# Kernel optimization log

Measured on AMD Instinct MI355X. Metric: run time of the kernel, lower is better.

The kernel has to match this reference:

```python
import jax, jax.numpy as jnp
import numpy as np

N_QUBITS = 10
N_LAYERS = 4
BATCH = 8192
DIM = 2 ** N_QUBITS


def setup_inputs() -> dict:
    key = jax.random.key(0)
    k1, k2 = jax.random.split(key)
    x = jax.random.normal(k1, (BATCH, N_QUBITS), dtype=jnp.float32)
    weights = jax.random.normal(k2, (N_LAYERS, N_QUBITS, 3), dtype=jnp.float32) * 0.1
    return {"x": x, "weights": weights}


def _apply_1q(state, U, q):
    """Apply shared 2x2 gate U to qubit q (wire 0 = most significant bit)."""
    B = state.shape[0]
    s = state.reshape(B, 2 ** q, 2, -1)
    s = jnp.einsum('ij,bajc->baic', U, s)
    return s.reshape(B, -1)


def _apply_1q_batched(state, U, q):
    """Apply per-sample 2x2 gates U[b] to qubit q."""
    B = state.shape[0]
    s = state.reshape(B, 2 ** q, 2, -1)
    s = jnp.einsum('bij,bajc->baic', U, s)
    return s.reshape(B, -1)


def _apply_cnot(state, c, t):
    """CNOT with control c, target t."""
    B = state.shape[0]
    s = state.reshape((B,) + (2,) * N_QUBITS)
    c_ax, t_ax = c + 1, t + 1
    ctrl0 = jnp.take(s, 0, axis=c_ax)
    ctrl1 = jnp.take(s, 1, axis=c_ax)
    # after removing control axis, target axis shifts down if it was after control
    t_ax2 = t_ax - 1 if t_ax > c_ax else t_ax
    ctrl1 = jnp.flip(ctrl1, axis=t_ax2)  # X on target when control=1
    s = jnp.stack([ctrl0, ctrl1], axis=c_ax)
    return s.reshape(B, -1)


def _rot_matrix(phi, theta, omega):
    """PennyLane Rot(phi,theta,omega) = RZ(omega) RY(theta) RZ(phi)."""
    c = jnp.cos(theta / 2)
    s = jnp.sin(theta / 2)
    e = lambda a: jnp.exp(1j * a)
    row0 = jnp.stack([e(-(phi + omega) / 2) * c, -e((phi - omega) / 2) * s])
    row1 = jnp.stack([e(-(phi - omega) / 2) * s, e((phi + omega) / 2) * c])
    return jnp.stack([row0, row1]).astype(jnp.complex64)


def _circuit(x, weights):
    B = x.shape[0]
    state = jnp.zeros((B, DIM), jnp.complex64).at[:, 0].set(1.0)
    # angle encoding: RY(x[:, q]) on each wire, batched over samples
    for q in range(N_QUBITS):
        a = x[:, q] / 2
        c, s = jnp.cos(a), jnp.sin(a)
        U = jnp.stack([jnp.stack([c, -s], -1), jnp.stack([s, c], -1)], -2)
        state = _apply_1q_batched(state, U.astype(jnp.complex64), q)
    for l in range(N_LAYERS):
        for q in range(N_QUBITS):
            U = _rot_matrix(weights[l, q, 0], weights[l, q, 1], weights[l, q, 2])
            state = _apply_1q(state, U, q)
        for q in range(N_QUBITS - 1):
            state = _apply_cnot(state, q, q + 1)
        if N_QUBITS > 2:
            state = _apply_cnot(state, N_QUBITS - 1, 0)
    # <Z_q> = sum_{bit_q=0} |amp|^2 - sum_{bit_q=1} |amp|^2
    probs = jnp.real(state) ** 2 + jnp.imag(state) ** 2
    outs = []
    for q in range(N_QUBITS):
        p = probs.reshape(B, 2 ** q, 2, -1)
        outs.append(p[:, :, 0, :].sum((1, 2)) - p[:, :, 1, :].sum((1, 2)))
    return jnp.stack(outs, axis=-1)  # [B, n_qubits]


def reference(x, weights):
    return _circuit(x, weights)
```

## Files before the change

### kernel.cpp

```cpp
#include <hip/hip_runtime.h>
#include <math.h>

#define NQ 10
#define NL 4

typedef float v2f __attribute__((ext_vector_type(2)));

template<int CTRL>
__device__ __forceinline__ float dppx(float v) {
  return __int_as_float(__builtin_amdgcn_update_dpp(0, __float_as_int(v), CTRL, 0xF, 0xF, true));
}
template<int OFF>
__device__ __forceinline__ float swzx(float v) {
  return __int_as_float(__builtin_amdgcn_ds_swizzle(__float_as_int(v), OFF));
}
__device__ __forceinline__ void pl16swap(float &a, float &b) {
  asm("v_permlane16_swap_b32 %0, %1" : "+v"(a), "+v"(b));
}
__device__ __forceinline__ void pl32swap(float &a, float &b) {
  asm("v_permlane32_swap_b32 %0, %1" : "+v"(a), "+v"(b));
}

template<int LB>
__device__ __forceinline__ float part(float v) {
  if constexpr (LB == 0) return dppx<0xB1>(v);
  else if constexpr (LB == 1) return dppx<0x4E>(v);
  else if constexpr (LB == 2) return swzx<0x101F>(v);
  else return swzx<0x201F>(v);
}

__device__ __forceinline__ v2f cmul(v2f u, v2f a) {
  v2f d;
  asm("v_pk_mul_f32 %0, %1, %2 op_sel_hi:[0,1]\n\t"
      "v_pk_fma_f32 %0, %1, %2, %0 op_sel:[1,1,0] op_sel_hi:[1,0,1] neg_lo:[0,1,0]"
      : "=&v"(d) : "v"(u), "v"(a));
  return d;
}
__device__ __forceinline__ void cfma(v2f &d, v2f u, v2f a) {
  asm("v_pk_fma_f32 %0, %1, %2, %0 op_sel_hi:[0,1,1]\n\t"
      "v_pk_fma_f32 %0, %1, %2, %0 op_sel:[1,1,0] op_sel_hi:[1,0,1] neg_lo:[0,1,0]"
      : "+v"(d) : "v"(u), "v"(a));
}

template<int RB>
__device__ __forceinline__ void gate_rbit(v2f a[16], v2f u00, v2f u01, v2f u10, v2f u11) {
#pragma unroll
  for (int r0 = 0; r0 < 16; ++r0) {
    if ((r0 >> RB) & 1) continue;
    const int r1 = r0 | (1 << RB);
    const v2f a0 = a[r0], a1 = a[r1];
    v2f n0 = cmul(u00, a0); cfma(n0, u01, a1);
    v2f n1 = cmul(u10, a0); cfma(n1, u11, a1);
    a[r0] = n0;
    a[r1] = n1;
  }
}

template<int LB>
__device__ __forceinline__ void gate_part(v2f a[16], v2f cS, v2f cP) {
#pragma unroll
  for (int h = 0; h < 4; ++h) {
    v2f p[4];
#pragma unroll
    for (int k = 0; k < 4; ++k) {
      const int r = h * 4 + k;
      p[k].x = part<LB>(a[r].x);
      p[k].y = part<LB>(a[r].y);
    }
#pragma unroll
    for (int k = 0; k < 4; ++k) {
      const int r = h * 4 + k;
      v2f n = cmul(cS, a[r]); cfma(n, cP, p[k]);
      a[r] = n;
    }
  }
}

template<bool IS32>
__device__ __forceinline__ void gate_swap(v2f a[16], v2f cL, v2f cH) {
#pragma unroll
  for (int r = 0; r < 16; ++r) {
    float lx = a[r].x, hx = a[r].x;
    float ly = a[r].y, hy = a[r].y;
    if constexpr (IS32) { pl32swap(lx, hx); pl32swap(ly, hy); }
    else                { pl16swap(lx, hx); pl16swap(ly, hy); }
    v2f lo, hi;
    lo.x = lx; lo.y = ly;
    hi.x = hx; hi.y = hy;
    v2f n = cmul(cL, lo); cfma(n, cH, hi);
    a[r] = n;
  }
}

__device__ __forceinline__ void ring_comp(v2f a[16], int addr0, int addr1, bool odd) {
  float B[16];
#pragma unroll
  for (int g = 0; g < 16; ++g) {
    const int par = ((g ^ (g >> 1) ^ (g >> 2) ^ (g >> 3)) & 1);
    B[g] = __int_as_float(__builtin_amdgcn_ds_bpermute(par ? addr1 : addr0,
                                                       __float_as_int(a[g].x)));
  }
#pragma unroll
  for (int r = 0; r < 16; ++r) {
    const int g = (r ^ (r >> 1));
    a[r].x = odd ? B[g ^ 12] : B[g];
  }
#pragma unroll
  for (int g = 0; g < 16; ++g) {
    const int par = ((g ^ (g >> 1) ^ (g >> 2) ^ (g >> 3)) & 1);
    B[g] = __int_as_float(__builtin_amdgcn_ds_bpermute(par ? addr1 : addr0,
                                                       __float_as_int(a[g].y)));
  }
#pragma unroll
  for (int r = 0; r < 16; ++r) {
    const int g = (r ^ (r >> 1));
    a[r].y = odd ? B[g ^ 12] : B[g];
  }
}

__device__ __forceinline__ float wsum(float v) {
  v += dppx<0xB1>(v);
  v += dppx<0x4E>(v);
  v += swzx<0x101F>(v);
  v += swzx<0x201F>(v);
  { float a = v, b = v; pl16swap(a, b); v = a + b; }
  { float a = v, b = v; pl32swap(a, b); v = a + b; }
  return v;
}

__device__ __forceinline__ void encode(const float* __restrict__ xb, int lane, v2f a[16]) {
  float lfac;
  {
    float c, s;
    sincosf(0.5f * xb[9], &s, &c); lfac  = ((lane >> 0) & 1) ? s : c;
    sincosf(0.5f * xb[8], &s, &c); lfac *= ((lane >> 1) & 1) ? s : c;
    sincosf(0.5f * xb[7], &s, &c); lfac *= ((lane >> 2) & 1) ? s : c;
    sincosf(0.5f * xb[6], &s, &c); lfac *= ((lane >> 3) & 1) ? s : c;
    sincosf(0.5f * xb[5], &s, &c); lfac *= ((lane >> 4) & 1) ? s : c;
    sincosf(0.5f * xb[4], &s, &c); lfac *= ((lane >> 5) & 1) ? s : c;
  }
  float c0, s0, c1, s1, c2, s2, c3, s3;
  sincosf(0.5f * xb[0], &s0, &c0);
  sincosf(0.5f * xb[1], &s1, &c1);
  sincosf(0.5f * xb[2], &s2, &c2);
  sincosf(0.5f * xb[3], &s3, &c3);
#pragma unroll
  for (int r = 0; r < 16; ++r) {
    float f = lfac;
    f *= ((r >> 0) & 1) ? s3 : c3;
    f *= ((r >> 1) & 1) ? s2 : c2;
    f *= ((r >> 2) & 1) ? s1 : c1;
    f *= ((r >> 3) & 1) ? s0 : c0;
    a[r].x = f;
    a[r].y = 0.f;
  }
}

__device__ __forceinline__ void measure(const v2f a[16], int lane, float z[NQ]) {
  float p[16];
#pragma unroll
  for (int r = 0; r < 16; ++r) p[r] = a[r].x * a[r].x + a[r].y * a[r].y;
#pragma unroll
  for (int q = 0; q < 4; ++q) {
    const int rb = 3 - q;
    float acc = 0.f;
#pragma unroll
    for (int r = 0; r < 16; ++r) acc += ((r >> rb) & 1) ? -p[r] : p[r];
    z[q] = acc;
  }
  float P = 0.f;
#pragma unroll
  for (int r = 0; r < 16; ++r) P += p[r];
#pragma unroll
  for (int q = 4; q < NQ; ++q) {
    const int lb = 9 - q;
    z[q] = ((lane >> lb) & 1) ? -P : P;
  }
#pragma unroll
  for (int q = 0; q < NQ; ++q) z[q] = wsum(z[q]);
}

__global__ __launch_bounds__(256) void qsim_kernel(const float* __restrict__ x,
                                                   const float* __restrict__ w,
                                                   float* __restrict__ out,
                                                   int batch) {
  __shared__ __align__(16) float gsh[NL * NQ * 8];
  const int tid = threadIdx.x;
  if (tid < NL * NQ) {
    const float phi = w[tid * 3 + 0];
    const float th  = w[tid * 3 + 1];
    const float om  = w[tid * 3 + 2];
    float c, s, cp, sp, cm, sm;
    sincosf(0.5f * th, &s, &c);
    sincosf(-0.5f * (phi + om), &sp, &cp);
    sincosf(0.5f * (phi - om), &sm, &cm);
    float* g = &gsh[tid * 8];
    g[0] = cp * c;  g[1] = sp * c;
    g[2] = -cm * s; g[3] = -sm * s;
    g[4] = cm * s;  g[5] = -sm * s;
    g[6] = cp * c;  g[7] = -sp * c;
  }
  __syncthreads();

  const int samp = (int)(blockIdx.x * (blockDim.x >> 6)) + (tid >> 6);
  const int lane = tid & 63;
  if (samp >= batch) return;

  const int addr0 = 4 * (lane ^ (lane >> 1));
  const int addr1 = addr0 ^ 128;
  const bool lodd = (lane & 1);

  v2f a[16];
  encode(x + samp * NQ, lane, a);

#pragma unroll
  for (int l = 0; l < NL; ++l) {
    const float* gl = &gsh[l * NQ * 8];

#pragma unroll
    for (int q = 0; q < 4; ++q) {
      const v2f* gv = (const v2f*)(gl + q * 8);
      const v2f u00 = gv[0], u01 = gv[1], u10 = gv[2], u11 = gv[3];
      if (q == 0)      gate_rbit<3>(a, u00, u01, u10, u11);
      else if (q == 1) gate_rbit<2>(a, u00, u01, u10, u11);
      else if (q == 2) gate_rbit<1>(a, u00, u01, u10, u11);
      else             gate_rbit<0>(a, u00, u01, u10, u11);
    }
    {
      const v2f* gv = (const v2f*)(gl + 4 * 8);
      const bool hb = (lane >> 5) & 1;
      const v2f cL = hb ? gv[2] : gv[0];
      const v2f cH = hb ? gv[3] : gv[1];
      gate_swap<true>(a, cL, cH);
    }
    {
      const v2f* gv = (const v2f*)(gl + 5 * 8);
      const bool hb = (lane >> 4) & 1;
      const v2f cL = hb ? gv[2] : gv[0];
      const v2f cH = hb ? gv[3] : gv[1];
      gate_swap<false>(a, cL, cH);
    }
#pragma unroll
    for (int q = 6; q < 10; ++q) {
      const v2f* gv = (const v2f*)(gl + q * 8);
      const bool hb = (lane >> (9 - q)) & 1;
      const v2f cS = hb ? gv[3] : gv[0];
      const v2f cP = hb ? gv[2] : gv[1];
      if (q == 6)      gate_part<3>(a, cS, cP);
      else if (q == 7) gate_part<2>(a, cS, cP);
      else if (q == 8) gate_part<1>(a, cS, cP);
      else             gate_part<0>(a, cS, cP);
    }

    ring_comp(a, addr0, addr1, lodd);
  }

  float z[NQ];
  measure(a, lane, z);

  if (lane == 0) {
#pragma unroll
    for (int q = 0; q < NQ; ++q) out[samp * NQ + q] = z[q];
  }
}

extern "C" void kernel_launch(void* const* d_in, const int* in_sizes, int n_in,
                              void* d_out, int out_size, void* d_ws, size_t ws_size,
                              hipStream_t stream) {
  const float* x = (const float*)d_in[0];
  const float* w = (const float*)d_in[1];
  float* out = (float*)d_out;
  const int batch = in_sizes[0] / NQ;
  const int waves_per_block = 256 / 64;
  const int grid = (batch + waves_per_block - 1) / waves_per_block;
  hipLaunchKernelGGL(qsim_kernel, dim3(grid), dim3(256), 0, stream, x, w, out, batch);
}
```

Before: 137.5 us.

## Precompute gates in separate kernel, use fast trig, merge lane-bit reductions

Moves the weight-to-gate-matrix computation into a tiny separate kernel that writes a global device array, so the main kernel no longer needs shared memory or __syncthreads and each block skips the redundant setup. Replaces sincosf with the fast __sinf/__cosf intrinsics in encoding and gate preparation. Replaces six separate wave reductions for the lane-bit qubits with a single butterfly reduction whose signed FMAs leave each qubit's expectation in a power-of-two lane. The trade-offs are reduced trig precision, an extra kernel launch, and gate coefficients now read from global memory instead of LDS.

New measurement: 147.1 us. 1.07x slower.

```diff
diff --git a/kernel.cpp b/kernel.cpp
--- a/kernel.cpp
+++ b/kernel.cpp
@@ -5,6 +5,8 @@
 #define NL 4
 
 typedef float v2f __attribute__((ext_vector_type(2)));
+
+__device__ float g_gates[NL * NQ * 8];
 
 template<int CTRL>
 __device__ __forceinline__ float dppx(float v) {
@@ -131,19 +133,19 @@
 __device__ __forceinline__ void encode(const float* __restrict__ xb, int lane, v2f a[16]) {
   float lfac;
   {
-    float c, s;
-    sincosf(0.5f * xb[9], &s, &c); lfac  = ((lane >> 0) & 1) ? s : c;
-    sincosf(0.5f * xb[8], &s, &c); lfac *= ((lane >> 1) & 1) ? s : c;
-    sincosf(0.5f * xb[7], &s, &c); lfac *= ((lane >> 2) & 1) ? s : c;
-    sincosf(0.5f * xb[6], &s, &c); lfac *= ((lane >> 3) & 1) ? s : c;
-    sincosf(0.5f * xb[5], &s, &c); lfac *= ((lane >> 4) & 1) ? s : c;
-    sincosf(0.5f * xb[4], &s, &c); lfac *= ((lane >> 5) & 1) ? s : c;
-  }
-  float c0, s0, c1, s1, c2, s2, c3, s3;
-  sincosf(0.5f * xb[0], &s0, &c0);
-  sincosf(0.5f * xb[1], &s1, &c1);
-  sincosf(0.5f * xb[2], &s2, &c2);
-  sincosf(0.5f * xb[3], &s3, &c3);
+    float c, s, h;
+    h = 0.5f * xb[9]; s = __sinf(h); c = __cosf(h); lfac  = ((lane >> 0) & 1) ? s : c;
+    h = 0.5f * xb[8]; s = __sinf(h); c = __cosf(h); lfac *= ((lane >> 1) & 1) ? s : c;
+    h = 0.5f * xb[7]; s = __sinf(h); c = __cosf(h); lfac *= ((lane >> 2) & 1) ? s : c;
+    h = 0.5f * xb[6]; s = __sinf(h); c = __cosf(h); lfac *= ((lane >> 3) & 1) ? s : c;
+    h = 0.5f * xb[5]; s = __sinf(h); c = __cosf(h); lfac *= ((lane >> 4) & 1) ? s : c;
+    h = 0.5f * xb[4]; s = __sinf(h); c = __cosf(h); lfac *= ((lane >> 5) & 1) ? s : c;
+  }
+  const float h0 = 0.5f * xb[0], h1 = 0.5f * xb[1], h2 = 0.5f * xb[2], h3 = 0.5f * xb[3];
+  const float s0 = __sinf(h0), c0 = __cosf(h0);
+  const float s1 = __sinf(h1), c1 = __cosf(h1);
+  const float s2 = __sinf(h2), c2 = __cosf(h2);
+  const float s3 = __sinf(h3), c3 = __cosf(h3);
 #pragma unroll
   for (int r = 0; r < 16; ++r) {
     float f = lfac;
@@ -156,52 +158,27 @@
   }
 }
 
-__device__ __forceinline__ void measure(const v2f a[16], int lane, float z[NQ]) {
-  float p[16];
-#pragma unroll
-  for (int r = 0; r < 16; ++r) p[r] = a[r].x * a[r].x + a[r].y * a[r].y;
-#pragma unroll
-  for (int q = 0; q < 4; ++q) {
-    const int rb = 3 - q;
-    float acc = 0.f;
-#pragma unroll
-    for (int r = 0; r < 16; ++r) acc += ((r >> rb) & 1) ? -p[r] : p[r];
-    z[q] = acc;
-  }
-  float P = 0.f;
-#pragma unroll
-  for (int r = 0; r < 16; ++r) P += p[r];
-#pragma unroll
-  for (int q = 4; q < NQ; ++q) {
-    const int lb = 9 - q;
-    z[q] = ((lane >> lb) & 1) ? -P : P;
-  }
-#pragma unroll
-  for (int q = 0; q < NQ; ++q) z[q] = wsum(z[q]);
-}
-
-__global__ __launch_bounds__(256) void qsim_kernel(const float* __restrict__ x,
-                                                   const float* __restrict__ w,
-                                                   float* __restrict__ out,
-                                                   int batch) {
-  __shared__ __align__(16) float gsh[NL * NQ * 8];
-  const int tid = threadIdx.x;
-  if (tid < NL * NQ) {
-    const float phi = w[tid * 3 + 0];
-    const float th  = w[tid * 3 + 1];
-    const float om  = w[tid * 3 + 2];
-    float c, s, cp, sp, cm, sm;
-    sincosf(0.5f * th, &s, &c);
-    sincosf(-0.5f * (phi + om), &sp, &cp);
-    sincosf(0.5f * (phi - om), &sm, &cm);
-    float* g = &gsh[tid * 8];
+__global__ void prep_gates(const float* __restrict__ w) {
+  const int t = threadIdx.x;
+  if (t < NL * NQ) {
+    const float phi = w[t * 3 + 0];
+    const float th  = w[t * 3 + 1];
+    const float om  = w[t * 3 + 2];
+    const float c  = __cosf(0.5f * th),          s  = __sinf(0.5f * th);
+    const float cp = __cosf(-0.5f * (phi + om)), sp = __sinf(-0.5f * (phi + om));
+    const float cm = __cosf(0.5f * (phi - om)),  sm = __sinf(0.5f * (phi - om));
+    float* g = g_gates + t * 8;
     g[0] = cp * c;  g[1] = sp * c;
     g[2] = -cm * s; g[3] = -sm * s;
     g[4] = cm * s;  g[5] = -sm * s;
     g[6] = cp * c;  g[7] = -sp * c;
   }
-  __syncthreads();
-
+}
+
+__global__ __launch_bounds__(256) void qsim_kernel(const float* __restrict__ x,
+                                                   float* __restrict__ out,
+                                                   int batch) {
+  const int tid = threadIdx.x;
   const int samp = (int)(blockIdx.x * (blockDim.x >> 6)) + (tid >> 6);
   const int lane = tid & 63;
   if (samp >= batch) return;
@@ -215,37 +192,44 @@
 
 #pragma unroll
   for (int l = 0; l < NL; ++l) {
-    const float* gl = &gsh[l * NQ * 8];
+    const float* gl = g_gates + l * NQ * 8;
 
 #pragma unroll
     for (int q = 0; q < 4; ++q) {
-      const v2f* gv = (const v2f*)(gl + q * 8);
-      const v2f u00 = gv[0], u01 = gv[1], u10 = gv[2], u11 = gv[3];
+      const float* g = gl + q * 8;
+      const v2f u00 = {g[0], g[1]}, u01 = {g[2], g[3]};
+      const v2f u10 = {g[4], g[5]}, u11 = {g[6], g[7]};
       if (q == 0)      gate_rbit<3>(a, u00, u01, u10, u11);
       else if (q == 1) gate_rbit<2>(a, u00, u01, u10, u11);
       else if (q == 2) gate_rbit<1>(a, u00, u01, u10, u11);
       else             gate_rbit<0>(a, u00, u01, u10, u11);
     }
     {
-      const v2f* gv = (const v2f*)(gl + 4 * 8);
+      const float* g = gl + 4 * 8;
       const bool hb = (lane >> 5) & 1;
-      const v2f cL = hb ? gv[2] : gv[0];
-      const v2f cH = hb ? gv[3] : gv[1];
+      const v2f u00 = {g[0], g[1]}, u01 = {g[2], g[3]};
+      const v2f u10 = {g[4], g[5]}, u11 = {g[6], g[7]};
+      const v2f cL = hb ? u10 : u00;
+      const v2f cH = hb ? u11 : u01;
       gate_swap<true>(a, cL, cH);
     }
     {
-      const v2f* gv = (const v2f*)(gl + 5 * 8);
+      const float* g = gl + 5 * 8;
       const bool hb = (lane >> 4) & 1;
-      const v2f cL = hb ? gv[2] : gv[0];
-      const v2f cH = hb ? gv[3] : gv[1];
+      const v2f u00 = {g[0], g[1]}, u01 = {g[2], g[3]};
+      const v2f u10 = {g[4], g[5]}, u11 = {g[6], g[7]};
+      const v2f cL = hb ? u10 : u00;
+      const v2f cH = hb ? u11 : u01;
       gate_swap<false>(a, cL, cH);
     }
 #pragma unroll
     for (int q = 6; q < 10; ++q) {
-      const v2f* gv = (const v2f*)(gl + q * 8);
+      const float* g = gl + q * 8;
       const bool hb = (lane >> (9 - q)) & 1;
-      const v2f cS = hb ? gv[3] : gv[0];
-      const v2f cP = hb ? gv[2] : gv[1];
+      const v2f u00 = {g[0], g[1]}, u01 = {g[2], g[3]};
+      const v2f u10 = {g[4], g[5]}, u11 = {g[6], g[7]};
+      const v2f cS = hb ? u11 : u00;
+      const v2f cP = hb ? u10 : u01;
       if (q == 6)      gate_part<3>(a, cS, cP);
       else if (q == 7) gate_part<2>(a, cS, cP);
       else if (q == 8) gate_part<1>(a, cS, cP);
@@ -255,12 +239,45 @@
     ring_comp(a, addr0, addr1, lodd);
   }
 
-  float z[NQ];
-  measure(a, lane, z);
+  float p[16];
+#pragma unroll
+  for (int r = 0; r < 16; ++r) p[r] = a[r].x * a[r].x + a[r].y * a[r].y;
+
+  float z03[4];
+#pragma unroll
+  for (int q = 0; q < 4; ++q) {
+    const int rb = 3 - q;
+    float acc = 0.f;
+#pragma unroll
+    for (int r = 0; r < 16; ++r) acc += ((r >> rb) & 1) ? -p[r] : p[r];
+    z03[q] = wsum(acc);
+  }
+
+  float P = 0.f;
+#pragma unroll
+  for (int r = 0; r < 16; ++r) P += p[r];
+  const float sg0 = (lane & 1)  ? -1.f : 1.f;
+  const float sg1 = (lane & 2)  ? -1.f : 1.f;
+  const float sg2 = (lane & 4)  ? -1.f : 1.f;
+  const float sg3 = (lane & 8)  ? -1.f : 1.f;
+  const float sg4 = (lane & 16) ? -1.f : 1.f;
+  const float sg5 = (lane & 32) ? -1.f : 1.f;
+  float v = P;
+  v = __builtin_fmaf(sg0, v, dppx<0xB1>(v));
+  v = __builtin_fmaf(sg1, v, dppx<0x4E>(v));
+  v = __builtin_fmaf(sg2, v, swzx<0x101F>(v));
+  v = __builtin_fmaf(sg3, v, swzx<0x201F>(v));
+  { float xx = v, yy = v; pl16swap(xx, yy); v = __builtin_fmaf(sg4, yy, xx); }
+  { float xx = v, yy = v; pl32swap(xx, yy); v = __builtin_fmaf(sg5, yy, xx); }
 
   if (lane == 0) {
-#pragma unroll
-    for (int q = 0; q < NQ; ++q) out[samp * NQ + q] = z[q];
+    out[samp * NQ + 0] = z03[0];
+    out[samp * NQ + 1] = z03[1];
+    out[samp * NQ + 2] = z03[2];
+    out[samp * NQ + 3] = z03[3];
+  } else if ((lane & (lane - 1)) == 0) {
+    const int lb = __ffs(lane) - 1;
+    out[samp * NQ + (9 - lb)] = v;
   }
 }
 
@@ -271,7 +288,10 @@
   const float* w = (const float*)d_in[1];
   float* out = (float*)d_out;
   const int batch = in_sizes[0] / NQ;
+
+  hipLaunchKernelGGL(prep_gates, dim3(1), dim3(64), 0, stream, w);
+
   const int waves_per_block = 256 / 64;
   const int grid = (batch + waves_per_block - 1) / waves_per_block;
-  hipLaunchKernelGGL(qsim_kernel, dim3(grid), dim3(256), 0, stream, x, w, out, batch);
-}
+  hipLaunchKernelGGL(qsim_kernel, dim3(grid), dim3(256), 0, stream, x, out, batch);
+}
```
